# Performance work log

Hardware: AMD Instinct MI355X
Metric: run time of the kernel (lower is better)

## Reference

```python
import jax, jax.numpy as jnp
import numpy as np


def setup_inputs() -> dict:
    key = jax.random.key(0)
    k1, k2, k3 = jax.random.split(key, 3)
    B, C, H, W = 4, 256, 64, 64
    K = max(C // 16, 8)  # 16
    x = jax.random.normal(k1, (B, C, H, W), dtype=jnp.float32)
    # conv1: 1x1 conv C -> K, i.e. a channel matmul with bias
    w1 = jax.random.normal(k2, (K, C), dtype=jnp.float32) * (1.0 / np.sqrt(C))
    b1 = jax.random.normal(k3, (K,), dtype=jnp.float32) * 0.01
    return {"x": x, "w1": w1, "b1": b1}


def reference(x, w1, b1):
    B, C, H, W = x.shape
    N = H * W
    xf = x.reshape(B, C, N)                       # [B, C, N]
    # conv1(x) flattened: proj used as both query and key (same weights)
    f = jnp.einsum('kc,bcn->bkn', w1, xf) + b1[None, :, None]  # [B, K, N]
    # energy[b, n, m] = sum_k f[b,k,n] * f[b,k,m]
    energy = jnp.einsum('bkn,bkm->bnm', f, f)     # [B, N, N]
    attention = jax.nn.softmax(energy, axis=-1)   # softmax over m
    # out[b,c,n] = sum_m value[b,c,m] * attention[b,n,m]
    out = jnp.einsum('bcm,bnm->bcn', xf, attention)
    out = out.reshape(B, C, H, W)
    return x + out * 0.1
```

## Files before the change

### kernel.cpp

```cpp
#include <hip/hip_runtime.h>
#include <hip/hip_bf16.h>

#define B_ 4
#define C_ 256
#define N_ 4096
#define K_ 16
#define QB 64
#define FSCALE 1.2011224087864498f
#define EXPA 8388608.0f
#define EXPB 1065101558.0f

typedef float f32x4 __attribute__((ext_vector_type(4)));
typedef float f32x16 __attribute__((ext_vector_type(16)));
typedef short s16x8 __attribute__((ext_vector_type(8)));
typedef int   i32x4 __attribute__((ext_vector_type(4)));
typedef int   i32x2 __attribute__((ext_vector_type(2)));

__device__ __forceinline__ short f2bf(float f) {
  union { float f; unsigned u; } v; v.f = f;
  unsigned r = v.u + 0x7fffu + ((v.u >> 16) & 1u);
  return (short)(r >> 16);
}
__device__ __forceinline__ int packbf(float a, float b) {
  __hip_bfloat162 h = __float22bfloat162_rn(make_float2(a, b));
  int r; __builtin_memcpy(&r, &h, 4); return r;
}

__global__ __launch_bounds__(256) void pre(const float* __restrict__ x,
                                           const float* __restrict__ w1,
                                           const float* __restrict__ b1,
                                           short* __restrict__ fT,
                                           short* __restrict__ vtP) {
  __shared__ __align__(16) char sm[20480];
  const int tid = threadIdx.x;
  if (blockIdx.x < 512) {
    float* w1t = (float*)sm;
    __shared__ float pr[8][32][17];
    for (int i = tid; i < C_ * K_; i += 256) {
      int k = i >> 8, c = i & 255;
      w1t[c * K_ + k] = w1[i];
    }
    __syncthreads();
    const int blk = blockIdx.x;
    const int b = blk >> 7;
    const int n0 = (blk & 127) * 32;
    const int nl = tid & 31;
    const int cch = tid >> 5;
    const int n = n0 + nl;
    const float* xp = x + (size_t)b * C_ * N_ + n;
    float acc[K_];
#pragma unroll
    for (int k = 0; k < K_; k++) acc[k] = 0.f;
    for (int cc = 0; cc < 32; cc++) {
      int c = cch * 32 + cc;
      float v = xp[(size_t)c * N_];
      const f32x4* wp = (const f32x4*)(&w1t[c * K_]);
#pragma unroll
      for (int qq = 0; qq < 4; qq++) {
        f32x4 wv = wp[qq];
#pragma unroll
        for (int j = 0; j < 4; j++) acc[qq * 4 + j] += wv[j] * v;
      }
    }
#pragma unroll
    for (int k = 0; k < K_; k++) pr[cch][nl][k] = acc[k];
    __syncthreads();
#pragma unroll
    for (int jj = 0; jj < 2; jj++) {
      int o = tid + jj * 256;
      int on = o >> 4, ok = o & 15;
      float s = b1[ok];
#pragma unroll
      for (int u = 0; u < 8; u++) s += pr[u][on][ok];
      fT[((size_t)b * N_ + n0 + on) * K_ + ok] = f2bf(s * FSCALE);
    }
  } else {
    short* t = (short*)sm;
    const int bid = blockIdx.x - 512;
    const int b = bid >> 7, cb = (bid >> 5) & 3, nb = bid & 31;
    const int n0 = nb * 128, c0 = cb * 64;
    const int r = tid >> 2, cg = tid & 3;
    const float* xp = x + ((size_t)(b * 256 + c0 + r)) * N_ + n0 + cg * 32;
#pragma unroll
    for (int k = 0; k < 8; k++) {
      f32x4 v = *(const f32x4*)(xp + k * 4);
      i32x2 p = {packbf(v[0], v[1]), packbf(v[2], v[3])};
      int col = (cg * 32 + k * 4) ^ ((r & 7) * 8);
      *(i32x2*)(&t[r * 136 + col]) = p;
    }
    __syncthreads();
#pragma unroll
    for (int u = 0; u < 4; u++) {
      int chunk = tid + 256 * u;
      int gl = chunk >> 6, c = chunk & 63;
      int m16 = gl >> 1, hi = gl & 1;
      int swz = (c & 7) * 8;
      i32x2 a = *(const i32x2*)(&t[c * 136 + ((m16 * 16 + hi * 4) ^ swz)]);
      i32x2 bq = *(const i32x2*)(&t[c * 136 + ((m16 * 16 + 8 + hi * 4) ^ swz)]);
      i32x4 vv = {a[0], a[1], bq[0], bq[1]};
      size_t g = (size_t)b * 512 + (size_t)(nb * 8 + m16) * 2 + hi;
      *(i32x4*)(vtP + (g * 256 + c0 + c) * 8) = vv;
    }
  }
}

__global__ __launch_bounds__(1024) void flash17(const float* __restrict__ x,
                                                const short* __restrict__ vtP,
                                                const short* __restrict__ fT,
                                                float* __restrict__ out) {
  __shared__ __align__(16) char lds[65536];
  const int tid = threadIdx.x;
  const int l = tid & 63;
  const int w = tid >> 6;
  const int h = w >> 3;
  const int u = w & 7;
  const int mt_p = u >> 1;
  const int nt_p = u & 1;
  const int hi = l >> 5;
  const int q = l & 31;
  const int id = blockIdx.x;
  const int b = id & 3;
  const int n0 = (id >> 2) * QB;

  const short* fTb = fT + (size_t)b * N_ * K_;
  const int mh0 = h * 2048;

  const s16x8 qf = *(const s16x8*)(fTb + (size_t)(n0 + nt_p * 32 + q) * K_ + hi * 8);
  const short* pkb = fTb + (size_t)(mh0 + mt_p * 64 + q) * K_ + hi * 8;
  const short* pvb = vtP + (((size_t)b * 512 + (mh0 >> 4) * 2 + hi) * 256 + u * 32 + q) * 8;

  char* pwr = lds + ((h * 2 + nt_p) * 4 + mt_p) * 4096 + hi * 512 + q * 16;
  const int prdO = hi * 512 + q * 16;

  f32x16 zero16 = {};
  f32x16 acc0 = zero16, acc1 = zero16;
  float lrun = 0.f;

  {
    s16x8 k0 = *(const s16x8*)(pkb);
    s16x8 k1 = *(const s16x8*)(pkb + 32 * K_);
    f32x16 st0 = __builtin_amdgcn_mfma_f32_32x32x16_bf16(k0, qf, zero16, 0, 0, 0);
    f32x16 st1 = __builtin_amdgcn_mfma_f32_32x32x16_bf16(k1, qf, zero16, 0, 0, 0);
    int sd0[8], sd1[8];
    float ps0 = 0.f, ps1 = 0.f, ps2 = 0.f, ps3 = 0.f;
#pragma unroll
    for (int s2 = 0; s2 < 8; s2++) {
      int ia = (int)(st0[2 * s2] * EXPA + EXPB);
      int ib = (int)(st0[2 * s2 + 1] * EXPA + EXPB);
      ps0 += __int_as_float(ia);
      ps1 += __int_as_float(ib);
      sd0[s2] = (int)__builtin_amdgcn_perm((unsigned)ib, (unsigned)ia, 0x07060302u);
    }
#pragma unroll
    for (int s2 = 0; s2 < 8; s2++) {
      int ia = (int)(st1[2 * s2] * EXPA + EXPB);
      int ib = (int)(st1[2 * s2 + 1] * EXPA + EXPB);
      ps2 += __int_as_float(ia);
      ps3 += __int_as_float(ib);
      sd1[s2] = (int)__builtin_amdgcn_perm((unsigned)ib, (unsigned)ia, 0x07060302u);
    }
    lrun += (ps0 + ps1) + (ps2 + ps3);
    *(i32x4*)(pwr)        = (i32x4){sd0[0], sd0[1], sd0[2], sd0[3]};
    *(i32x4*)(pwr + 1024) = (i32x4){sd0[4], sd0[5], sd0[6], sd0[7]};
    *(i32x4*)(pwr + 2048) = (i32x4){sd1[0], sd1[1], sd1[2], sd1[3]};
    *(i32x4*)(pwr + 3072) = (i32x4){sd1[4], sd1[5], sd1[6], sd1[7]};
  }
  __syncthreads();
  s16x8 kf0 = *(const s16x8*)(pkb + 256 * K_);
  s16x8 kf1 = *(const s16x8*)(pkb + 256 * K_ + 32 * K_);

  for (int si = 0; si < 8; ++si) {
    const float lsc = (si < 7) ? 1.f : 0.f;
    const short* pkn = pkb + (size_t)((si + 2 < 7 ? si + 2 : 7) * 256) * K_;

    __builtin_amdgcn_s_setprio(1);

    f32x16 st0 = __builtin_amdgcn_mfma_f32_32x32x16_bf16(kf0, qf, zero16, 0, 0, 0);
    f32x16 st1 = __builtin_amdgcn_mfma_f32_32x32x16_bf16(kf1, qf, zero16, 0, 0, 0);
    s16x8 nk0 = *(const s16x8*)(pkn);
    s16x8 nk1 = *(const s16x8*)(pkn + 32 * K_);
    int sd0[8], sd1[8];
    float ps0 = 0.f, ps1 = 0.f, ps2 = 0.f, ps3 = 0.f;
#pragma unroll
    for (int s2 = 0; s2 < 8; s2++) {
      int ia = (int)(st0[2 * s2] * EXPA + EXPB);
      int ib = (int)(st0[2 * s2 + 1] * EXPA + EXPB);
      ps0 += __int_as_float(ia);
      ps1 += __int_as_float(ib);
      sd0[s2] = (int)__builtin_amdgcn_perm((unsigned)ib, (unsigned)ia, 0x07060302u);
    }
#pragma unroll
    for (int s2 = 0; s2 < 8; s2++) {
      int ia = (int)(st1[2 * s2] * EXPA + EXPB);
      int ib = (int)(st1[2 * s2 + 1] * EXPA + EXPB);
      ps2 += __int_as_float(ia);
      ps3 += __int_as_float(ib);
      sd1[s2] = (int)__builtin_amdgcn_perm((unsigned)ib, (unsigned)ia, 0x07060302u);
    }
    lrun += lsc * ((ps0 + ps1) + (ps2 + ps3));

#pragma unroll
    for (int mt = 0; mt < 4; ++mt) {
      const short* pv = pvb + (size_t)(si * 4 + mt) * 16384;
      s16x8 vA0 = *(const s16x8*)(pv);
      s16x8 vA1 = *(const s16x8*)(pv + 4096);
      s16x8 vA2 = *(const s16x8*)(pv + 8192);
      s16x8 vA3 = *(const s16x8*)(pv + 12288);
      const char* p0 = lds + ((h * 2 + 0) * 4 + mt) * 4096 + prdO;
      const char* p1 = lds + ((h * 2 + 1) * 4 + mt) * 4096 + prdO;
      s16x8 pa0 = __builtin_bit_cast(s16x8, *(const i32x4*)(p0));
      s16x8 pb0 = __builtin_bit_cast(s16x8, *(const i32x4*)(p1));
      acc0 = __builtin_amdgcn_mfma_f32_32x32x16_bf16(vA0, pa0, acc0, 0, 0, 0);
      acc1 = __builtin_amdgcn_mfma_f32_32x32x16_bf16(vA0, pb0, acc1, 0, 0, 0);
      s16x8 pa1 = __builtin_bit_cast(s16x8, *(const i32x4*)(p0 + 1024));
      s16x8 pb1 = __builtin_bit_cast(s16x8, *(const i32x4*)(p1 + 1024));
      acc0 = __builtin_amdgcn_mfma_f32_32x32x16_bf16(vA1, pa1, acc0, 0, 0, 0);
      acc1 = __builtin_amdgcn_mfma_f32_32x32x16_bf16(vA1, pb1, acc1, 0, 0, 0);
      s16x8 pa2 = __builtin_bit_cast(s16x8, *(const i32x4*)(p0 + 2048));
      s16x8 pb2 = __builtin_bit_cast(s16x8, *(const i32x4*)(p1 + 2048));
      acc0 = __builtin_amdgcn_mfma_f32_32x32x16_bf16(vA2, pa2, acc0, 0, 0, 0);
      acc1 = __builtin_amdgcn_mfma_f32_32x32x16_bf16(vA2, pb2, acc1, 0, 0, 0);
      s16x8 pa3 = __builtin_bit_cast(s16x8, *(const i32x4*)(p0 + 3072));
      s16x8 pb3 = __builtin_bit_cast(s16x8, *(const i32x4*)(p1 + 3072));
      acc0 = __builtin_amdgcn_mfma_f32_32x32x16_bf16(vA3, pa3, acc0, 0, 0, 0);
      acc1 = __builtin_amdgcn_mfma_f32_32x32x16_bf16(vA3, pb3, acc1, 0, 0, 0);
    }
    __builtin_amdgcn_s_setprio(0);
    __syncthreads();

    *(i32x4*)(pwr)        = (i32x4){sd0[0], sd0[1], sd0[2], sd0[3]};
    *(i32x4*)(pwr + 1024) = (i32x4){sd0[4], sd0[5], sd0[6], sd0[7]};
    *(i32x4*)(pwr + 2048) = (i32x4){sd1[0], sd1[1], sd1[2], sd1[3]};
    *(i32x4*)(pwr + 3072) = (i32x4){sd1[4], sd1[5], sd1[6], sd1[7]};
    __syncthreads();

    kf0 = nk0; kf1 = nk1;
  }

  lrun += __shfl_xor(lrun, 32);

  float* mlb = (float*)lds;
  mlb[w * 64 + l] = lrun;
  __syncthreads();
  float L0 = 0.f, L1 = 0.f;
#pragma unroll
  for (int hh = 0; hh < 2; ++hh)
#pragma unroll
    for (int mt = 0; mt < 4; ++mt) {
      L0 += mlb[(hh * 8 + mt * 2 + 0) * 64 + l];
      L1 += mlb[(hh * 8 + mt * 2 + 1) * 64 + l];
    }
  __syncthreads();
  char* xch = lds;
  const int xbase = (u * 64 + l) * 128;
  if (h == 1) {
#pragma unroll
    for (int i = 0; i < 8; i++) {
      f32x4 v;
#pragma unroll
      for (int r = 0; r < 4; r++) v[r] = (i >> 2) ? acc1[(i & 3) * 4 + r] : acc0[(i & 3) * 4 + r];
      *(f32x4*)(xch + xbase + ((i * 16) ^ ((l & 7) << 4))) = v;
    }
  }
  __syncthreads();
  if (h == 0) {
    const float inv0 = 0.1f / L0;
    const float inv1 = 0.1f / L1;
#pragma unroll
    for (int i = 0; i < 8; i++) {
      f32x4 po = *(const f32x4*)(xch + xbase + ((i * 16) ^ ((l & 7) << 4)));
      const int p_ = i & 3;
      const int ntw = i >> 2;
      const float inv = ntw ? inv1 : inv0;
      const int n = n0 + ntw * 32 + q;
      const int cbase = u * 32 + p_ * 8 + hi * 4;
#pragma unroll
      for (int r = 0; r < 4; r++) {
        const float own = ntw ? acc1[p_ * 4 + r] : acc0[p_ * 4 + r];
        const size_t idx = ((size_t)b * C_ + (cbase + r)) * N_ + n;
        out[idx] = x[idx] + (own + po[r]) * inv;
      }
    }
  }
}

extern "C" void kernel_launch(void* const* d_in, const int* in_sizes, int n_in,
                              void* d_out, int out_size, void* d_ws, size_t ws_size,
                              hipStream_t stream) {
  const float* x  = (const float*)d_in[0];
  const float* w1 = (const float*)d_in[1];
  const float* b1 = (const float*)d_in[2];
  float* out = (float*)d_out;
  short* fT  = (short*)d_ws;
  short* vtP = (short*)((char*)d_ws + 512 * 1024);
  pre<<<dim3(1024), dim3(256), 0, stream>>>(x, w1, b1, fT, vtP);
  flash17<<<dim3(256), dim3(1024), 0, stream>>>(x, vtP, fT, out);
}
```

Baseline: 61.38 us.

## Fuse projection and V transpose in pre, prefetch V tiles, use LDS-only barriers

The pre kernel now reads each x tile once, computing the 1x1 projection and writing the bf16 swizzled V layout from the same load. Before, separate block groups each read x. The launch shrinks to 256 larger blocks. In the flash kernel, the first V fragment group of the next step is prefetched into registers across the loop iteration, and the two __syncthreads are replaced by barriers that wait only on LDS counters, so outstanding global loads can stay in flight. This raises register pressure and lowers parallelism in the pre kernel.

```diff
diff --git a/kernel.cpp b/kernel.cpp
--- a/kernel.cpp
+++ b/kernel.cpp
@@ -21,9 +21,12 @@
   unsigned r = v.u + 0x7fffu + ((v.u >> 16) & 1u);
   return (short)(r >> 16);
 }
-__device__ __forceinline__ int packbf(float a, float b) {
-  __hip_bfloat162 h = __float22bfloat162_rn(make_float2(a, b));
-  int r; __builtin_memcpy(&r, &h, 4); return r;
+
+__device__ __forceinline__ void bar_lds_only() {
+  asm volatile("s_waitcnt lgkmcnt(0)" ::: "memory");
+  __builtin_amdgcn_sched_barrier(0);
+  __builtin_amdgcn_s_barrier();
+  __builtin_amdgcn_sched_barrier(0);
 }
 
 __global__ __launch_bounds__(256) void pre(const float* __restrict__ x,
@@ -31,80 +34,64 @@
                                            const float* __restrict__ b1,
                                            short* __restrict__ fT,
                                            short* __restrict__ vtP) {
-  __shared__ __align__(16) char sm[20480];
+  __shared__ __align__(16) char sm[50176];
+  short* t   = (short*)sm;
+  float* w1t = (float*)(sm + 32768);
+  float* pr  = (float*)(sm + 32768);
   const int tid = threadIdx.x;
-  if (blockIdx.x < 512) {
-    float* w1t = (float*)sm;
-    __shared__ float pr[8][32][17];
-    for (int i = tid; i < C_ * K_; i += 256) {
-      int k = i >> 8, c = i & 255;
-      w1t[c * K_ + k] = w1[i];
-    }
-    __syncthreads();
-    const int blk = blockIdx.x;
-    const int b = blk >> 7;
-    const int n0 = (blk & 127) * 32;
-    const int nl = tid & 31;
-    const int cch = tid >> 5;
-    const int n = n0 + nl;
-    const float* xp = x + (size_t)b * C_ * N_ + n;
-    float acc[K_];
-#pragma unroll
-    for (int k = 0; k < K_; k++) acc[k] = 0.f;
-    for (int cc = 0; cc < 32; cc++) {
-      int c = cch * 32 + cc;
-      float v = xp[(size_t)c * N_];
-      const f32x4* wp = (const f32x4*)(&w1t[c * K_]);
-#pragma unroll
-      for (int qq = 0; qq < 4; qq++) {
-        f32x4 wv = wp[qq];
-#pragma unroll
-        for (int j = 0; j < 4; j++) acc[qq * 4 + j] += wv[j] * v;
-      }
-    }
-#pragma unroll
-    for (int k = 0; k < K_; k++) pr[cch][nl][k] = acc[k];
-    __syncthreads();
-#pragma unroll
-    for (int jj = 0; jj < 2; jj++) {
-      int o = tid + jj * 256;
-      int on = o >> 4, ok = o & 15;
-      float s = b1[ok];
-#pragma unroll
-      for (int u = 0; u < 8; u++) s += pr[u][on][ok];
-      fT[((size_t)b * N_ + n0 + on) * K_ + ok] = f2bf(s * FSCALE);
-    }
-  } else {
-    short* t = (short*)sm;
-    const int bid = blockIdx.x - 512;
-    const int b = bid >> 7, cb = (bid >> 5) & 3, nb = bid & 31;
-    const int n0 = nb * 128, c0 = cb * 64;
-    const int r = tid >> 2, cg = tid & 3;
-    const float* xp = x + ((size_t)(b * 256 + c0 + r)) * N_ + n0 + cg * 32;
-#pragma unroll
-    for (int k = 0; k < 8; k++) {
-      f32x4 v = *(const f32x4*)(xp + k * 4);
-      i32x2 p = {packbf(v[0], v[1]), packbf(v[2], v[3])};
-      int col = (cg * 32 + k * 4) ^ ((r & 7) * 8);
-      *(i32x2*)(&t[r * 136 + col]) = p;
-    }
-    __syncthreads();
-#pragma unroll
-    for (int u = 0; u < 4; u++) {
-      int chunk = tid + 256 * u;
-      int gl = chunk >> 6, c = chunk & 63;
-      int m16 = gl >> 1, hi = gl & 1;
-      int swz = (c & 7) * 8;
-      i32x2 a = *(const i32x2*)(&t[c * 136 + ((m16 * 16 + hi * 4) ^ swz)]);
-      i32x2 bq = *(const i32x2*)(&t[c * 136 + ((m16 * 16 + 8 + hi * 4) ^ swz)]);
+  const int b = blockIdx.x >> 6;
+  const int n0 = (blockIdx.x & 63) * 64;
+  for (int i = tid; i < C_ * K_; i += 256) {
+    int k = i >> 8, c = i & 255;
+    w1t[c * K_ + k] = w1[i];
+  }
+  __syncthreads();
+  const int nl = tid & 63;
+  const int cch = tid >> 6;
+  const float* xp = x + ((size_t)b * C_ + cch * 64) * N_ + n0 + nl;
+  float acc[K_];
+#pragma unroll
+  for (int k = 0; k < K_; k++) acc[k] = 0.f;
+  for (int cc = 0; cc < 64; cc++) {
+    const int c = cch * 64 + cc;
+    float v = xp[(size_t)cc * N_];
+    t[c * 64 + (nl ^ ((c & 7) * 8))] = f2bf(v);
+    const f32x4* wp = (const f32x4*)(&w1t[c * K_]);
+#pragma unroll
+    for (int qq = 0; qq < 4; qq++) {
+      f32x4 wv = wp[qq];
+#pragma unroll
+      for (int j = 0; j < 4; j++) acc[qq * 4 + j] += wv[j] * v;
+    }
+  }
+  __syncthreads();
+#pragma unroll
+  for (int k = 0; k < K_; k++) pr[(cch * 64 + nl) * 17 + k] = acc[k];
+  __syncthreads();
+#pragma unroll
+  for (int jj = 0; jj < 4; jj++) {
+    int o = tid + jj * 256;
+    int on = o >> 4, ok = o & 15;
+    float s = b1[ok] + pr[(0 * 64 + on) * 17 + ok] + pr[(1 * 64 + on) * 17 + ok] +
+              pr[(2 * 64 + on) * 17 + ok] + pr[(3 * 64 + on) * 17 + ok];
+    fT[((size_t)b * N_ + n0 + on) * K_ + ok] = f2bf(s * FSCALE);
+  }
+  {
+    const int c = tid;
+    const int swz = (c & 7) * 8;
+#pragma unroll
+    for (int g = 0; g < 8; g++) {
+      const int m16 = g >> 1, hi = g & 1;
+      i32x2 a  = *(const i32x2*)(&t[c * 64 + ((m16 * 16 + hi * 4) ^ swz)]);
+      i32x2 bq = *(const i32x2*)(&t[c * 64 + ((m16 * 16 + 8 + hi * 4) ^ swz)]);
       i32x4 vv = {a[0], a[1], bq[0], bq[1]};
-      size_t g = (size_t)b * 512 + (size_t)(nb * 8 + m16) * 2 + hi;
-      *(i32x4*)(vtP + (g * 256 + c0 + c) * 8) = vv;
-    }
-  }
-}
-
-__global__ __launch_bounds__(1024) void flash17(const float* __restrict__ x,
+      const size_t gg = (size_t)b * 512 + (n0 >> 3) + m16 * 2 + hi;
+      *(i32x4*)(vtP + (gg * 256 + c) * 8) = vv;
+    }
+  }
+}
+
+__global__ __launch_bounds__(1024) void flash18(const float* __restrict__ x,
                                                 const short* __restrict__ vtP,
                                                 const short* __restrict__ fT,
                                                 float* __restrict__ out) {
@@ -168,10 +155,15 @@
   __syncthreads();
   s16x8 kf0 = *(const s16x8*)(pkb + 256 * K_);
   s16x8 kf1 = *(const s16x8*)(pkb + 256 * K_ + 32 * K_);
+  s16x8 vc0 = *(const s16x8*)(pvb);
+  s16x8 vc1 = *(const s16x8*)(pvb + 4096);
+  s16x8 vc2 = *(const s16x8*)(pvb + 8192);
+  s16x8 vc3 = *(const s16x8*)(pvb + 12288);
 
   for (int si = 0; si < 8; ++si) {
     const float lsc = (si < 7) ? 1.f : 0.f;
     const short* pkn = pkb + (size_t)((si + 2 < 7 ? si + 2 : 7) * 256) * K_;
+    const short* pvn = pvb + (size_t)((si < 7 ? si + 1 : 7) * 4) * 16384;
 
     __builtin_amdgcn_s_setprio(1);
 
@@ -179,6 +171,10 @@
     f32x16 st1 = __builtin_amdgcn_mfma_f32_32x32x16_bf16(kf1, qf, zero16, 0, 0, 0);
     s16x8 nk0 = *(const s16x8*)(pkn);
     s16x8 nk1 = *(const s16x8*)(pkn + 32 * K_);
+    s16x8 nv0 = *(const s16x8*)(pvn);
+    s16x8 nv1 = *(const s16x8*)(pvn + 4096);
+    s16x8 nv2 = *(const s16x8*)(pvn + 8192);
+    s16x8 nv3 = *(const s16x8*)(pvn + 12288);
     int sd0[8], sd1[8];
     float ps0 = 0.f, ps1 = 0.f, ps2 = 0.f, ps3 = 0.f;
 #pragma unroll
@@ -201,11 +197,16 @@
 
 #pragma unroll
     for (int mt = 0; mt < 4; ++mt) {
-      const short* pv = pvb + (size_t)(si * 4 + mt) * 16384;
-      s16x8 vA0 = *(const s16x8*)(pv);
-      s16x8 vA1 = *(const s16x8*)(pv + 4096);
-      s16x8 vA2 = *(const s16x8*)(pv + 8192);
-      s16x8 vA3 = *(const s16x8*)(pv + 12288);
+      s16x8 vA0, vA1, vA2, vA3;
+      if (mt == 0) {
+        vA0 = vc0; vA1 = vc1; vA2 = vc2; vA3 = vc3;
+      } else {
+        const short* pv = pvb + (size_t)(si * 4 + mt) * 16384;
+        vA0 = *(const s16x8*)(pv);
+        vA1 = *(const s16x8*)(pv + 4096);
+        vA2 = *(const s16x8*)(pv + 8192);
+        vA3 = *(const s16x8*)(pv + 12288);
+      }
       const char* p0 = lds + ((h * 2 + 0) * 4 + mt) * 4096 + prdO;
       const char* p1 = lds + ((h * 2 + 1) * 4 + mt) * 4096 + prdO;
       s16x8 pa0 = __builtin_bit_cast(s16x8, *(const i32x4*)(p0));
@@ -226,15 +227,18 @@
       acc1 = __builtin_amdgcn_mfma_f32_32x32x16_bf16(vA3, pb3, acc1, 0, 0, 0);
     }
     __builtin_amdgcn_s_setprio(0);
-    __syncthreads();
+
+    bar_lds_only();
 
     *(i32x4*)(pwr)        = (i32x4){sd0[0], sd0[1], sd0[2], sd0[3]};
     *(i32x4*)(pwr + 1024) = (i32x4){sd0[4], sd0[5], sd0[6], sd0[7]};
     *(i32x4*)(pwr + 2048) = (i32x4){sd1[0], sd1[1], sd1[2], sd1[3]};
     *(i32x4*)(pwr + 3072) = (i32x4){sd1[4], sd1[5], sd1[6], sd1[7]};
-    __syncthreads();
+
+    bar_lds_only();
 
     kf0 = nk0; kf1 = nk1;
+    vc0 = nv0; vc1 = nv1; vc2 = nv2; vc3 = nv3;
   }
 
   lrun += __shfl_xor(lrun, 32);
@@ -293,6 +297,6 @@
   float* out = (float*)d_out;
   short* fT  = (short*)d_ws;
   short* vtP = (short*)((char*)d_ws + 512 * 1024);
-  pre<<<dim3(1024), dim3(256), 0, stream>>>(x, w1, b1, fT, vtP);
-  flash17<<<dim3(256), dim3(1024), 0, stream>>>(x, vtP, fT, out);
-}
+  pre<<<dim3(256), dim3(256), 0, stream>>>(x, w1, b1, fT, vtP);
+  flash18<<<dim3(256), dim3(1024), 0, stream>>>(x, vtP, fT, out);
+}
```

After: 70.46 us. +14.8%, slower.
